# Performance work log

Measured on AMD Instinct MI355X. Metric: run time of the kernel, lower is better.

## Reference

```python
import jax, jax.numpy as jnp
import numpy as np

N = 200000   # nodes (Elliptic-scale)
E = 500000   # directed edges
F = 166      # in_channels / node feature dim
H = 128      # hidden_channels
C = 2        # out_channels
T = 49       # number of time steps


def setup_inputs() -> dict:
    key = jax.random.key(0)
    ks = jax.random.split(key, 12)
    x = jax.random.normal(ks[0], (N, F), jnp.float32)
    edge_index = jax.random.randint(ks[1], (2, E), 0, N, dtype=jnp.int32)
    time_step = jax.random.randint(ks[2], (N,), 0, T, dtype=jnp.int32)
    sF = 1.0 / np.sqrt(F)
    sH = 1.0 / np.sqrt(H)
    initial_w = jax.random.uniform(ks[3], (F, F), jnp.float32, -sF, sF)
    gru_w_ih = jax.random.uniform(ks[4], (3 * F, F), jnp.float32, -sF, sF)
    gru_w_hh = jax.random.uniform(ks[5], (3 * F, F), jnp.float32, -sF, sF)
    gru_b_ih = jax.random.uniform(ks[6], (3 * F,), jnp.float32, -sF, sF)
    gru_b_hh = jax.random.uniform(ks[7], (3 * F,), jnp.float32, -sF, sF)
    proj_w = jax.random.uniform(ks[8], (H, F), jnp.float32, -sF, sF)
    proj_b = jax.random.uniform(ks[9], (H,), jnp.float32, -sF, sF)
    cls_w = jax.random.uniform(ks[10], (C, H), jnp.float32, -sH, sH)
    cls_b = jax.random.uniform(ks[11], (C,), jnp.float32, -sH, sH)
    return {"x": x, "edge_index": edge_index, "time_step": time_step,
            "initial_w": initial_w, "gru_w_ih": gru_w_ih, "gru_w_hh": gru_w_hh,
            "gru_b_ih": gru_b_ih, "gru_b_hh": gru_b_hh,
            "proj_w": proj_w, "proj_b": proj_b, "cls_w": cls_w, "cls_b": cls_b}


def reference(x, edge_index, time_step, initial_w, gru_w_ih, gru_w_hh,
              gru_b_ih, gru_b_hh, proj_w, proj_b, cls_w, cls_b):
    src, dst = edge_index[0], edge_index[1]
    n = x.shape[0]

    def gru(W):
        # torch.nn.GRU single step, input = hidden = W  (FxF matrix, rows = batch)
        gi = W @ gru_w_ih.T + gru_b_ih
        gh = W @ gru_w_hh.T + gru_b_hh
        i_r, i_z, i_n = jnp.split(gi, 3, axis=-1)
        h_r, h_z, h_n = jnp.split(gh, 3, axis=-1)
        r = jax.nn.sigmoid(i_r + h_r)
        z = jax.nn.sigmoid(i_z + h_z)
        nn_ = jnp.tanh(i_n + r * h_n)
        return (1.0 - z) * nn_ + z * W

    def step(carry, t):
        W, logits = carry
        W = gru(W)  # evolve GCN weight (EvolveGCN-O)
        # subgraph of nodes with time_step <= t, expressed by masking (same math
        # as relabel+extract: inactive nodes contribute nothing, their outputs are ignored)
        act = time_step <= t
        ew = (act[src] & act[dst]).astype(x.dtype)
        # gcn_norm with self-loops: deg = in-degree over active edges + 1
        deg = jax.ops.segment_sum(ew, dst, num_segments=n) + 1.0
        dinv = jax.lax.rsqrt(deg)
        norm = ew * dinv[src] * dinv[dst]
        h = jnp.where(act[:, None], x, 0.0) @ W               # [N, F]
        agg = jax.ops.segment_sum(h[src] * norm[:, None], dst, num_segments=n)
        agg = agg + h / deg[:, None]                          # self-loop term dinv_i^2 * h_i
        z = jax.nn.relu(agg @ proj_w.T + proj_b)              # [N, H] (dropout: eval mode)
        lg = z @ cls_w.T + cls_b                              # [N, C]
        logits = jnp.where((time_step == t)[:, None], lg, logits)
        return (W, logits), None

    init = (initial_w, jnp.zeros((n, cls_w.shape[0]), x.dtype))
    (_, logits), _ = jax.lax.scan(step, init, jnp.arange(T, dtype=time_step.dtype))
    return logits
```

## Files before the change

kernel.cpp:

```cpp
#include <hip/hip_runtime.h>
#include <hip/hip_fp16.h>
#include <math.h>

#define NN 200000
#define NE 500000
#define FF 166
#define HH 128
#define CC 2
#define TT 49
#define GG 498
#define PADN 203136
#define MAXTILES 6400
#define KP 84
#define KPAD 192
#define SCB 512
#define SNB 391
#define HB 782

typedef _Float16 half2v __attribute__((ext_vector_type(2)));
typedef _Float16 f16x8 __attribute__((ext_vector_type(8)));
typedef float f32x4 __attribute__((ext_vector_type(4)));

static __device__ __forceinline__ float fdot2f(half2v a, half2v b, float c) {
#if __has_builtin(__builtin_amdgcn_fdot2)
    return __builtin_amdgcn_fdot2(a, b, c, false);
#else
    return c + (float)a.x * (float)b.x + (float)a.y * (float)b.y;
#endif
}

__global__ void prep_pack(const float* __restrict__ wih, const float* __restrict__ whh,
                          const float* __restrict__ projw,
                          _Float16* __restrict__ wkp, float* __restrict__ projwT) {
    int idx = blockIdx.x * 256 + threadIdx.x;
    const int A = 2 * KP * 512;
    if (idx < A) {
        int m = idx / (KP * 512);
        int r = idx - m * (KP * 512);
        int kp = r >> 9, c = r & 511;
        const float* Wm = m ? whh : wih;
        float x0 = 0.0f, x1 = 0.0f;
        if (c < GG) {
            int k0 = 2 * kp, k1 = 2 * kp + 1;
            if (k0 < FF) x0 = Wm[c * FF + k0];
            if (k1 < FF) x1 = Wm[c * FF + k1];
        }
        wkp[2 * idx]     = (_Float16)x0;
        wkp[2 * idx + 1] = (_Float16)x1;
    } else if (idx < A + FF * HH) {
        int q = idx - A;
        int k = q >> 7, h = q & 127;
        projwT[q] = projw[h * FF + k];
    }
}

__global__ __launch_bounds__(256) void x_to_h(const float* __restrict__ x, half2v* __restrict__ x2) {
    int idx = blockIdx.x * 256 + threadIdx.x;
    if (idx >= NN * 96) return;
    int row = idx / 96, cp = idx - row * 96;
    int c0 = cp * 2;
    float v0 = (c0 < FF) ? x[(size_t)row * FF + c0] : 0.0f;
    float v1 = (c0 + 1 < FF) ? x[(size_t)row * FF + c0 + 1] : 0.0f;
    half2v h;
    h[0] = (_Float16)v0;
    h[1] = (_Float16)v1;
    x2[idx] = h;
}

__global__ void count_indeg(const int* __restrict__ dst, int* __restrict__ off) {
    int e = blockIdx.x * 256 + threadIdx.x;
    if (e < NE) atomicAdd(&off[dst[e]], 1);
}

__global__ __launch_bounds__(256) void scan_p1(const int* __restrict__ off, int* __restrict__ bsum) {
    __shared__ int s[256];
    int b = blockIdx.x, tid = threadIdx.x;
    int i0 = b * SCB + tid * 2;
    int v = 0;
    if (i0 < NN) v += off[i0];
    if (i0 + 1 < NN) v += off[i0 + 1];
    s[tid] = v;
    __syncthreads();
    for (int d = 128; d > 0; d >>= 1) {
        if (tid < d) s[tid] += s[tid + d];
        __syncthreads();
    }
    if (tid == 0) bsum[b] = s[0];
}

__global__ __launch_bounds__(512) void scan_p2(const int* __restrict__ bsum, int* __restrict__ bpre,
                                               int* __restrict__ off) {
    __shared__ int s[512];
    int tid = threadIdx.x;
    int v = (tid < SNB) ? bsum[tid] : 0;
    s[tid] = v;
    __syncthreads();
    for (int d = 1; d < 512; d <<= 1) {
        int u = (tid >= d) ? s[tid - d] : 0;
        __syncthreads();
        s[tid] += u;
        __syncthreads();
    }
    bpre[tid] = s[tid] - v;
    if (tid == 511) off[NN] = s[511];
}

__global__ __launch_bounds__(512) void scan_p3(int* __restrict__ off, const int* __restrict__ bpre) {
    __shared__ int s[512];
    int b = blockIdx.x, tid = threadIdx.x;
    int i = b * SCB + tid;
    int v = (i < NN) ? off[i] : 0;
    s[tid] = v;
    __syncthreads();
    for (int d = 1; d < 512; d <<= 1) {
        int u = (tid >= d) ? s[tid - d] : 0;
        __syncthreads();
        s[tid] += u;
        __syncthreads();
    }
    if (i < NN) off[i] = s[tid] - v + bpre[b];
}

__global__ void fill_adj(const int* __restrict__ src, const int* __restrict__ dst,
                         const int* __restrict__ off, int* __restrict__ cursor,
                         int* __restrict__ adjsrc, int* __restrict__ dstid) {
    int e = blockIdx.x * 256 + threadIdx.x;
    if (e < NE) {
        int d = dst[e];
        int p = atomicAdd(&cursor[d], 1);
        adjsrc[off[d] + p] = src[e];
        dstid[off[d] + p] = d;
    }
}

__global__ __launch_bounds__(256) void degf_hist(const int* __restrict__ off, const int* __restrict__ adjsrc,
                                                 const int* __restrict__ ts, _Float16* __restrict__ dinvh,
                                                 float* __restrict__ selfdeg) {
    __shared__ unsigned short sh[TT * 256];
    int tid = threadIdx.x;
    int i = blockIdx.x * 256 + tid;
    for (int t = 0; t < TT; ++t) sh[t * 256 + tid] = 0;
    if (i >= NN) return;
    int tsi = ts[i];
    int e0 = off[i], e1 = off[i + 1];
    for (int e = e0; e < e1; ++e) {
        int tj = ts[adjsrc[e]];
        sh[tj * 256 + tid]++;
    }
    int cum = 1;
    for (int t = 0; t < TT; ++t) {
        cum += sh[t * 256 + tid];
        dinvh[(size_t)t * NN + i] = (_Float16)rsqrtf((float)cum);
        if (t == tsi) selfdeg[i] = 1.0f / (float)cum;
    }
}

__global__ __launch_bounds__(256) void edge_prep(const int* __restrict__ adjsrc, const int* __restrict__ dstid,
                                                 const int* __restrict__ ts, const _Float16* __restrict__ dinvh,
                                                 int2* __restrict__ ewp) {
    int e = blockIdx.x * 256 + threadIdx.x;
    if (e >= NE) return;
    int j = adjsrc[e], i = dstid[e];
    int t = ts[i];
    float w = 0.0f;
    if (ts[j] <= t)
        w = (float)dinvh[(size_t)t * NN + j] * (float)dinvh[(size_t)t * NN + i];
    int2 p;
    p.x = j;
    p.y = __float_as_int(w);
    ewp[e] = p;
}

__global__ __launch_bounds__(256) void hist_rank(const int* __restrict__ ts,
                                                 int* __restrict__ cnt, int* __restrict__ rank) {
    __shared__ int h[TT];
    int tid = threadIdx.x, b = blockIdx.x;
    if (tid < TT) h[tid] = 0;
    __syncthreads();
    int i = b * 256 + tid;
    if (i < NN) {
        int t = ts[i];
        rank[i] = atomicAdd(&h[t], 1);
    }
    __syncthreads();
    if (tid < TT) cnt[b * TT + tid] = h[tid];
}

__global__ __launch_bounds__(256) void bucket_scan(const int* __restrict__ cnt,
                                                   int* __restrict__ basecol, int* __restrict__ bcnt) {
    __shared__ int s[256];
    int t = blockIdx.x, tid = threadIdx.x;
    const int CH = (HB + 255) / 256;
    int b0 = tid * CH;
    int loc[CH];
    int sum = 0;
    for (int u = 0; u < CH; ++u) {
        int b = b0 + u;
        int v = (b < HB) ? cnt[b * TT + t] : 0;
        loc[u] = sum;
        sum += v;
    }
    s[tid] = sum;
    __syncthreads();
    for (int d = 1; d < 256; d <<= 1) {
        int u = (tid >= d) ? s[tid - d] : 0;
        __syncthreads();
        s[tid] += u;
        __syncthreads();
    }
    int base = s[tid] - sum;
    for (int u = 0; u < CH; ++u) {
        int b = b0 + u;
        if (b < HB) basecol[b * TT + t] = base + loc[u];
    }
    if (tid == 255) bcnt[t] = s[255];
}

__global__ __launch_bounds__(256) void perm_scatter(const int* __restrict__ ts, const int* __restrict__ rank,
                                                    const int* __restrict__ basecol, const int* __restrict__ pstart,
                                                    int* __restrict__ perm) {
    int b = blockIdx.x;
    int i = b * 256 + threadIdx.x;
    if (i < NN) {
        int t = ts[i];
        perm[pstart[t] + basecol[b * TT + t] + rank[i]] = i;
    }
}

__global__ void make_tiles(const int* __restrict__ bcnt, int* __restrict__ pstart,
                           int* __restrict__ tile_t, int* __restrict__ tile_r0,
                           int* __restrict__ meta) {
    __shared__ int s_nt[64];
    int t = threadIdx.x;
    int nt = (t < TT) ? (bcnt[t] + 31) / 32 : 0;
    s_nt[t] = nt;
    __syncthreads();
    for (int d = 1; d < 64; d <<= 1) {
        int v = (t >= d) ? s_nt[t - d] : 0;
        __syncthreads();
        s_nt[t] += v;
        __syncthreads();
    }
    int ntbase = s_nt[t] - nt;
    int pbase = ntbase * 32;
    if (t < TT) {
        pstart[t] = pbase;
        for (int u = 0; u < nt; ++u) {
            tile_t[ntbase + u] = t;
            tile_r0[ntbase + u] = pbase + u * 32;
        }
    }
    if (t == 63) {
        meta[0] = s_nt[63];
        meta[1] = s_nt[63] * 32;
        pstart[TT] = s_nt[63] * 32;
    }
}

__global__ __launch_bounds__(512) void gru_evolve(
        const float* __restrict__ initial_w,
        const _Float16* __restrict__ wkp,
        const float* __restrict__ bih, const float* __restrict__ bhh,
        float* __restrict__ W_all) {
    __shared__ float s_w[FF];
    __shared__ __align__(16) _Float16 s_wh[2 * KP];
    __shared__ float s_pre[2][512];
    int tid = threadIdx.x;
    int row = blockIdx.x;

    if (tid < FF) {
        float v = initial_w[(size_t)row * FF + tid];
        s_w[tid] = v;
        s_wh[tid] = (_Float16)v;
    } else if (tid < 2 * KP) {
        s_wh[tid] = (_Float16)0.0f;
    }

    int cc0 = tid * 2;
    bool act = cc0 < 996;
    int m = (cc0 >= 498) ? 1 : 0;
    int c0 = act ? (cc0 - m * 498) : 0;

    half2v wr0[KP], wr1[KP];
    {
        const half2v* __restrict__ pW =
            (const half2v*)wkp + (size_t)(act ? m : 0) * (KP * 512) + c0;
        #pragma unroll
        for (int kp = 0; kp < KP; ++kp) {
            wr0[kp] = pW[(size_t)(kp << 9)];
            wr1[kp] = pW[(size_t)(kp << 9) + 1];
        }
    }

    float bi_r = 0, bi_z = 0, bi_n = 0, bh_r = 0, bh_z = 0, bh_n = 0;
    if (tid < FF) {
        bi_r = bih[tid]; bi_z = bih[FF + tid]; bi_n = bih[2 * FF + tid];
        bh_r = bhh[tid]; bh_z = bhh[FF + tid]; bh_n = bhh[2 * FF + tid];
    }
    __syncthreads();

    const f16x8* s_wh8 = (const f16x8*)s_wh;
    for (int t = 0; t < TT; ++t) {
        if (act) {
            float a0 = 0.0f, a1 = 0.0f;
            #pragma unroll
            for (int q = 0; q < 21; ++q) {
                f16x8 w8 = s_wh8[q];
                half2v h0 = __builtin_shufflevector(w8, w8, 0, 1);
                half2v h1 = __builtin_shufflevector(w8, w8, 2, 3);
                half2v h2 = __builtin_shufflevector(w8, w8, 4, 5);
                half2v h3 = __builtin_shufflevector(w8, w8, 6, 7);
                a0 = fdot2f(wr0[4 * q + 0], h0, a0);  a1 = fdot2f(wr1[4 * q + 0], h0, a1);
                a0 = fdot2f(wr0[4 * q + 1], h1, a0);  a1 = fdot2f(wr1[4 * q + 1], h1, a1);
                a0 = fdot2f(wr0[4 * q + 2], h2, a0);  a1 = fdot2f(wr1[4 * q + 2], h2, a1);
                a0 = fdot2f(wr0[4 * q + 3], h3, a0);  a1 = fdot2f(wr1[4 * q + 3], h3, a1);
            }
            s_pre[m][c0]     = a0;
            s_pre[m][c0 + 1] = a1;
        }
        __syncthreads();
        if (tid < FF) {
            float i_r = s_pre[0][tid]          + bi_r;
            float h_r = s_pre[1][tid]          + bh_r;
            float i_z = s_pre[0][FF + tid]     + bi_z;
            float h_z = s_pre[1][FF + tid]     + bh_z;
            float i_n = s_pre[0][2 * FF + tid] + bi_n;
            float h_n = s_pre[1][2 * FF + tid] + bh_n;
            float rg = 1.0f / (1.0f + expf(-(i_r + h_r)));
            float zg = 1.0f / (1.0f + expf(-(i_z + h_z)));
            float ng = tanhf(i_n + rg * h_n);
            float wnew = (1.0f - zg) * ng + zg * s_w[tid];
            s_w[tid] = wnew;
            s_wh[tid] = (_Float16)wnew;
            W_all[((size_t)t * FF + row) * FF + tid] = wnew;
        }
        __syncthreads();
    }
}

__global__ __launch_bounds__(1024) void m_build(const float* __restrict__ W_all,
                                                const float* __restrict__ projwT,
                                                _Float16* __restrict__ Mh) {
    __shared__ __align__(16) float sw[8][168];
    int blk = blockIdx.x;
    int t = blk / 24, rb = blk - t * 24;
    int tid = threadIdx.x;
    int r0 = rb * 8;
    for (int idx = tid; idx < 8 * FF; idx += 1024) {
        int rr = idx / FF, k = idx - rr * FF;
        int r = r0 + rr;
        sw[rr][k] = (r < FF) ? W_all[((size_t)t * FF + r) * FF + k] : 0.0f;
    }
    __syncthreads();
    int rr = tid >> 7, h = tid & 127;
    int r = r0 + rr;
    if (r >= KPAD) return;
    float acc = 0.0f;
    if (r < FF) {
        const float* __restrict__ pw = projwT + h;
        #pragma unroll 4
        for (int c4 = 0; c4 < 164; c4 += 4) {
            float4 w = *(const float4*)&sw[rr][c4];
            acc += w.x * pw[(size_t)(c4 + 0) << 7];
            acc += w.y * pw[(size_t)(c4 + 1) << 7];
            acc += w.z * pw[(size_t)(c4 + 2) << 7];
            acc += w.w * pw[(size_t)(c4 + 3) << 7];
        }
        acc += sw[rr][164] * pw[(size_t)164 << 7];
        acc += sw[rr][165] * pw[(size_t)165 << 7];
    }
    Mh[((size_t)t * HH + h) * KPAD + r] = (_Float16)acc;
}

__global__ __launch_bounds__(512) void gemm_fused3(
        const int* __restrict__ meta, const int* __restrict__ tile_t,
        const int* __restrict__ tile_r0, const int* __restrict__ perm,
        const float* __restrict__ selfdeg, const half2v* __restrict__ x2,
        const int* __restrict__ off, const int2* __restrict__ ewp,
        const _Float16* __restrict__ Mh, const float* __restrict__ proj_b,
        const float* __restrict__ cls_w, const float* __restrict__ cls_b,
        float* __restrict__ out) {
    __shared__ __align__(16) char smraw[32 * 130 * 4];
    _Float16* sY = (_Float16*)smraw;
    float* sP = (float*)smraw;
    int bid = blockIdx.x;
    if (bid >= meta[0]) return;
    int t = tile_t[bid], r0 = tile_r0[bid];
    int tid = threadIdx.x;
    int lane = tid & 63;
    int w = tid >> 6;
    bool lo = lane < 32;

    for (int q = 0; q < 4; ++q) {
        int rrow = w * 4 + q;
        int i = perm[r0 + rrow];
        float a0x = 0.f, a0y = 0.f, a1x = 0.f, a1y = 0.f;
        if (i >= 0) {
            float sw = selfdeg[i];
            const half2v* xi = x2 + (size_t)i * 96;
            half2v h0 = xi[lane];
            a0x = sw * (float)h0[0];
            a0y = sw * (float)h0[1];
            if (lo) {
                half2v h1 = xi[64 + lane];
                a1x = sw * (float)h1[0];
                a1y = sw * (float)h1[1];
            }
            int e0 = off[i], e1 = off[i + 1];
            for (int e = e0; e < e1; ++e) {
                int2 p = ewp[e];
                float wv = __int_as_float(p.y);
                if (wv != 0.0f) {
                    const half2v* xj = x2 + (size_t)p.x * 96;
                    half2v g0 = xj[lane];
                    a0x += wv * (float)g0[0];
                    a0y += wv * (float)g0[1];
                    if (lo) {
                        half2v g1 = xj[64 + lane];
                        a1x += wv * (float)g1[0];
                        a1y += wv * (float)g1[1];
                    }
                }
            }
        }
        half2v o0;
        o0[0] = (_Float16)a0x;
        o0[1] = (_Float16)a0y;
        *(half2v*)(sY + rrow * 200 + lane * 2) = o0;
        if (lo) {
            half2v o1;
            o1[0] = (_Float16)a1x;
            o1[1] = (_Float16)a1y;
            *(half2v*)(sY + rrow * 200 + 128 + lane * 2) = o1;
        }
    }
    __syncthreads();

    int lr = lane & 15;
    int kg = lane >> 4;
    int c0 = w * 16;
    f32x4 acc0 = {0, 0, 0, 0}, acc1 = {0, 0, 0, 0};
    const _Float16* B0 = Mh + ((size_t)t * HH + c0 + lr) * KPAD + kg * 8;
    const _Float16* A0 = sY + lr * 200 + kg * 8;
    const _Float16* A1 = A0 + 16 * 200;

    #pragma unroll
    for (int s = 0; s < 6; ++s) {
        f16x8 b0 = *(const f16x8*)(B0 + s * 32);
        f16x8 a0 = *(const f16x8*)(A0 + s * 32);
        f16x8 a1 = *(const f16x8*)(A1 + s * 32);
        acc0 = __builtin_amdgcn_mfma_f32_16x16x32_f16(a0, b0, acc0, 0, 0, 0);
        acc1 = __builtin_amdgcn_mfma_f32_16x16x32_f16(a1, b0, acc1, 0, 0, 0);
    }

    float pb = proj_b[c0 + lr];
    __syncthreads();
    int prow = kg * 4;
    int colw = c0 + lr;
    #pragma unroll
    for (int r = 0; r < 4; ++r) {
        sP[(prow + r) * 130 + colw]      = fmaxf(acc0[r] + pb, 0.0f);
        sP[(16 + prow + r) * 130 + colw] = fmaxf(acc1[r] + pb, 0.0f);
    }
    __syncthreads();

    int row = tid >> 4, cc = (tid >> 3) & 1, qq = tid & 7;
    const float* pr = sP + row * 130 + qq * 16;
    const float* cw = cls_w + cc * HH + qq * 16;
    float s = 0.0f;
    #pragma unroll
    for (int h = 0; h < 16; ++h) s += pr[h] * cw[h];
    s += __shfl_xor(s, 1);
    s += __shfl_xor(s, 2);
    s += __shfl_xor(s, 4);
    if (qq == 0) {
        int node = perm[r0 + row];
        if (node >= 0) out[(size_t)node * CC + cc] = s + cls_b[cc];
    }
}

extern "C" void kernel_launch(void* const* d_in, const int* in_sizes, int n_in,
                              void* d_out, int out_size, void* d_ws, size_t ws_size,
                              hipStream_t stream) {
    const float* x = (const float*)d_in[0];
    const int* ei = (const int*)d_in[1];
    const int* srcp = ei;
    const int* dstp = ei + NE;
    const int* ts = (const int*)d_in[2];
    const float* initial_w = (const float*)d_in[3];
    const float* wih = (const float*)d_in[4];
    const float* whh = (const float*)d_in[5];
    const float* bih = (const float*)d_in[6];
    const float* bhh = (const float*)d_in[7];
    const float* projw = (const float*)d_in[8];
    const float* projb = (const float*)d_in[9];
    const float* clsw = (const float*)d_in[10];
    const float* clsb = (const float*)d_in[11];
    float* out = (float*)d_out;

    char* base = (char*)d_ws;
    size_t o = 0;
    auto alloc = [&](size_t bytes) { size_t r = o; o = (o + bytes + 255) & ~(size_t)255; return r; };

    float*    W_all   = (float*)   (base + alloc((size_t)TT * FF * FF * 4));
    _Float16* Mh      = (_Float16*)(base + alloc((size_t)TT * HH * KPAD * 2));
    _Float16* wkp     = (_Float16*)(base + alloc((size_t)2 * KP * 512 * 2 * 2));
    float*    projwT  = (float*)   (base + alloc((size_t)FF * HH * 4));
    int*      off     = (int*)     (base + alloc((size_t)(NN + 1) * 4));
    int*      cursor  = (int*)     (base + alloc((size_t)NN * 4));
    int*      adjsrc  = (int*)     (base + alloc((size_t)NE * 4));
    int*      dstid   = (int*)     (base + alloc((size_t)NE * 4));
    int2*     ewp     = (int2*)    (base + alloc((size_t)NE * 8));
    _Float16* dinvh   = (_Float16*)(base + alloc((size_t)TT * NN * 2));
    float*    selfdeg = (float*)   (base + alloc((size_t)NN * 4));
    int*      bcnt    = (int*)     (base + alloc((size_t)TT * 4));
    int*      pstart  = (int*)     (base + alloc((size_t)(TT + 1) * 4));
    int*      meta    = (int*)     (base + alloc(2 * 4));
    int*      tile_t  = (int*)     (base + alloc((size_t)MAXTILES * 4));
    int*      tile_r0 = (int*)     (base + alloc((size_t)MAXTILES * 4));
    int*      perm    = (int*)     (base + alloc((size_t)PADN * 4));
    int*      bsum    = (int*)     (base + alloc((size_t)512 * 4));
    int*      bpre    = (int*)     (base + alloc((size_t)520 * 4));
    int*      cnt     = (int*)     (base + alloc((size_t)HB * TT * 4));
    int*      basecol = (int*)     (base + alloc((size_t)HB * TT * 4));
    int*      rank    = (int*)     (base + alloc((size_t)NN * 4));
    half2v*   x2      = (half2v*)  (base + alloc((size_t)NN * 96 * 4));

    hipMemsetAsync(off, 0, (size_t)(NN + 1) * 4, stream);
    hipMemsetAsync(cursor, 0, (size_t)NN * 4, stream);
    hipMemsetAsync(perm, 0xFF, (size_t)PADN * 4, stream);

    prep_pack<<<420, 256, 0, stream>>>(wih, whh, projw, wkp, projwT);
    x_to_h<<<(NN * 96 + 255) / 256, 256, 0, stream>>>(x, x2);
    count_indeg<<<(NE + 255) / 256, 256, 0, stream>>>(dstp, off);
    hist_rank<<<HB, 256, 0, stream>>>(ts, cnt, rank);
    scan_p1<<<SNB, 256, 0, stream>>>(off, bsum);
    scan_p2<<<1, 512, 0, stream>>>(bsum, bpre, off);
    scan_p3<<<SNB, 512, 0, stream>>>(off, bpre);
    fill_adj<<<(NE + 255) / 256, 256, 0, stream>>>(srcp, dstp, off, cursor, adjsrc, dstid);
    degf_hist<<<(NN + 255) / 256, 256, 0, stream>>>(off, adjsrc, ts, dinvh, selfdeg);
    edge_prep<<<(NE + 255) / 256, 256, 0, stream>>>(adjsrc, dstid, ts, dinvh, ewp);
    bucket_scan<<<TT, 256, 0, stream>>>(cnt, basecol, bcnt);
    make_tiles<<<1, 64, 0, stream>>>(bcnt, pstart, tile_t, tile_r0, meta);
    perm_scatter<<<HB, 256, 0, stream>>>(ts, rank, basecol, pstart, perm);

    gru_evolve<<<FF, 512, 0, stream>>>(initial_w, wkp, bih, bhh, W_all);
    m_build<<<TT * 24, 1024, 0, stream>>>(W_all, projwT, Mh);

    gemm_fused3<<<MAXTILES, 512, 0, stream>>>(meta, tile_t, tile_r0, perm, selfdeg,
                                              x2, off, ewp, Mh, projb, clsw, clsb, out);
}
```

Measured before the change: 392.6 us.

## Interleave edge gathers across four rows and cache source timesteps in CSR

The aggregation loop in the fused GEMM kernel now walks the edge lists of a wave's four rows together instead of one row at a time. This keeps up to four independent neighbour-feature gathers in flight per wave and hides gather latency. Separately, fill_adj stores each edge's source timestep into a CSR-ordered array, so degf_hist and edge_prep no longer do a dependent indirect lookup of ts[src]. The cost is more registers per thread, some wasted iterations when degrees are uneven, and one extra edge-sized buffer.

After: 391.1 us. No clear change (-0.4%).

```diff
diff --git a/kernel.cpp b/kernel.cpp
--- a/kernel.cpp
+++ b/kernel.cpp
@@ -122,18 +122,23 @@
 }
 
 __global__ void fill_adj(const int* __restrict__ src, const int* __restrict__ dst,
+                         const int* __restrict__ ts,
                          const int* __restrict__ off, int* __restrict__ cursor,
-                         int* __restrict__ adjsrc, int* __restrict__ dstid) {
+                         int* __restrict__ adjsrc, int* __restrict__ dstid,
+                         int* __restrict__ tsrc) {
     int e = blockIdx.x * 256 + threadIdx.x;
     if (e < NE) {
         int d = dst[e];
+        int s = src[e];
         int p = atomicAdd(&cursor[d], 1);
-        adjsrc[off[d] + p] = src[e];
-        dstid[off[d] + p] = d;
-    }
-}
-
-__global__ __launch_bounds__(256) void degf_hist(const int* __restrict__ off, const int* __restrict__ adjsrc,
+        int pos = off[d] + p;
+        adjsrc[pos] = s;
+        dstid[pos] = d;
+        tsrc[pos] = ts[s];
+    }
+}
+
+__global__ __launch_bounds__(256) void degf_hist(const int* __restrict__ off, const int* __restrict__ tsrc,
                                                  const int* __restrict__ ts, _Float16* __restrict__ dinvh,
                                                  float* __restrict__ selfdeg) {
     __shared__ unsigned short sh[TT * 256];
@@ -144,7 +149,7 @@
     int tsi = ts[i];
     int e0 = off[i], e1 = off[i + 1];
     for (int e = e0; e < e1; ++e) {
-        int tj = ts[adjsrc[e]];
+        int tj = tsrc[e];
         sh[tj * 256 + tid]++;
     }
     int cum = 1;
@@ -156,6 +161,7 @@
 }
 
 __global__ __launch_bounds__(256) void edge_prep(const int* __restrict__ adjsrc, const int* __restrict__ dstid,
+                                                 const int* __restrict__ tsrc,
                                                  const int* __restrict__ ts, const _Float16* __restrict__ dinvh,
                                                  int2* __restrict__ ewp) {
     int e = blockIdx.x * 256 + threadIdx.x;
@@ -163,7 +169,7 @@
     int j = adjsrc[e], i = dstid[e];
     int t = ts[i];
     float w = 0.0f;
-    if (ts[j] <= t)
+    if (tsrc[e] <= t)
         w = (float)dinvh[(size_t)t * NN + j] * (float)dinvh[(size_t)t * NN + i];
     int2 p;
     p.x = j;
@@ -391,47 +397,70 @@
     int w = tid >> 6;
     bool lo = lane < 32;
 
+    int rbase = w * 4;
+    int idx4[4], ep[4], ee[4];
+    float ax[4], ay[4], bx[4], by[4];
+    #pragma unroll
     for (int q = 0; q < 4; ++q) {
-        int rrow = w * 4 + q;
-        int i = perm[r0 + rrow];
-        float a0x = 0.f, a0y = 0.f, a1x = 0.f, a1y = 0.f;
+        int i = perm[r0 + rbase + q];
+        idx4[q] = i;
+        ax[q] = ay[q] = bx[q] = by[q] = 0.0f;
+        ep[q] = 0; ee[q] = 0;
+        if (i >= 0) { ep[q] = off[i]; ee[q] = off[i + 1]; }
+    }
+    #pragma unroll
+    for (int q = 0; q < 4; ++q) {
+        int i = idx4[q];
         if (i >= 0) {
             float sw = selfdeg[i];
             const half2v* xi = x2 + (size_t)i * 96;
             half2v h0 = xi[lane];
-            a0x = sw * (float)h0[0];
-            a0y = sw * (float)h0[1];
+            ax[q] = sw * (float)h0[0];
+            ay[q] = sw * (float)h0[1];
             if (lo) {
                 half2v h1 = xi[64 + lane];
-                a1x = sw * (float)h1[0];
-                a1y = sw * (float)h1[1];
+                bx[q] = sw * (float)h1[0];
+                by[q] = sw * (float)h1[1];
             }
-            int e0 = off[i], e1 = off[i + 1];
-            for (int e = e0; e < e1; ++e) {
-                int2 p = ewp[e];
-                float wv = __int_as_float(p.y);
-                if (wv != 0.0f) {
-                    const half2v* xj = x2 + (size_t)p.x * 96;
-                    half2v g0 = xj[lane];
-                    a0x += wv * (float)g0[0];
-                    a0y += wv * (float)g0[1];
-                    if (lo) {
-                        half2v g1 = xj[64 + lane];
-                        a1x += wv * (float)g1[0];
-                        a1y += wv * (float)g1[1];
-                    }
+        }
+    }
+    while ((ep[0] < ee[0]) | (ep[1] < ee[1]) | (ep[2] < ee[2]) | (ep[3] < ee[3])) {
+        float wv[4]; int js[4];
+        #pragma unroll
+        for (int q = 0; q < 4; ++q) {
+            wv[q] = 0.0f; js[q] = 0;
+            if (ep[q] < ee[q]) {
+                int2 p = ewp[ep[q]++];
+                js[q] = p.x;
+                wv[q] = __int_as_float(p.y);
+            }
+        }
+        #pragma unroll
+        for (int q = 0; q < 4; ++q) {
+            if (wv[q] != 0.0f) {
+                const half2v* xj = x2 + (size_t)js[q] * 96;
+                half2v g0 = xj[lane];
+                ax[q] += wv[q] * (float)g0[0];
+                ay[q] += wv[q] * (float)g0[1];
+                if (lo) {
+                    half2v g1 = xj[64 + lane];
+                    bx[q] += wv[q] * (float)g1[0];
+                    by[q] += wv[q] * (float)g1[1];
                 }
             }
         }
+    }
+    #pragma unroll
+    for (int q = 0; q < 4; ++q) {
         half2v o0;
-        o0[0] = (_Float16)a0x;
-        o0[1] = (_Float16)a0y;
-        *(half2v*)(sY + rrow * 200 + lane * 2) = o0;
+        o0[0] = (_Float16)ax[q];
+        o0[1] = (_Float16)ay[q];
+        *(half2v*)(sY + (rbase + q) * 200 + lane * 2) = o0;
         if (lo) {
             half2v o1;
-            o1[0] = (_Float16)a1x;
-            o1[1] = (_Float16)a1y;
-            *(half2v*)(sY + rrow * 200 + 128 + lane * 2) = o1;
+            o1[0] = (_Float16)bx[q];
+            o1[1] = (_Float16)by[q];
+            *(half2v*)(sY + (rbase + q) * 200 + 128 + lane * 2) = o1;
         }
     }
     __syncthreads();
@@ -510,6 +539,7 @@
     int*      cursor  = (int*)     (base + alloc((size_t)NN * 4));
     int*      adjsrc  = (int*)     (base + alloc((size_t)NE * 4));
     int*      dstid   = (int*)     (base + alloc((size_t)NE * 4));
+    int*      tsrc    = (int*)     (base + alloc((size_t)NE * 4));
     int2*     ewp     = (int2*)    (base + alloc((size_t)NE * 8));
     _Float16* dinvh   = (_Float16*)(base + alloc((size_t)TT * NN * 2));
     float*    selfdeg = (float*)   (base + alloc((size_t)NN * 4));
@@ -537,9 +567,9 @@
     scan_p1<<<SNB, 256, 0, stream>>>(off, bsum);
     scan_p2<<<1, 512, 0, stream>>>(bsum, bpre, off);
     scan_p3<<<SNB, 512, 0, stream>>>(off, bpre);
-    fill_adj<<<(NE + 255) / 256, 256, 0, stream>>>(srcp, dstp, off, cursor, adjsrc, dstid);
-    degf_hist<<<(NN + 255) / 256, 256, 0, stream>>>(off, adjsrc, ts, dinvh, selfdeg);
-    edge_prep<<<(NE + 255) / 256, 256, 0, stream>>>(adjsrc, dstid, ts, dinvh, ewp);
+    fill_adj<<<(NE + 255) / 256, 256, 0, stream>>>(srcp, dstp, ts, off, cursor, adjsrc, dstid, tsrc);
+    degf_hist<<<(NN + 255) / 256, 256, 0, stream>>>(off, tsrc, ts, dinvh, selfdeg);
+    edge_prep<<<(NE + 255) / 256, 256, 0, stream>>>(adjsrc, dstid, tsrc, ts, dinvh, ewp);
     bucket_scan<<<TT, 256, 0, stream>>>(cnt, basecol, bcnt);
     make_tiles<<<1, 64, 0, stream>>>(bcnt, pstart, tile_t, tile_r0, meta);
     perm_scatter<<<HB, 256, 0, stream>>>(ts, rank, basecol, pstart, perm);
```
